# Kernel tuning notes

Measured on AMD Instinct MI355X. Metric: run time of the kernel, lower is better.

Reference implementation:

```python
import jax, jax.numpy as jnp
import numpy as np
import math

D_MODEL = 1024
HEADS = 16
D_K = D_MODEL // HEADS
D_FF = 2048
EPS = 1e-6


def layer_norm(x, alpha, bias):
    # torch.std uses unbiased estimator (ddof=1)
    m = x.mean(axis=-1, keepdims=True)
    var = ((x - m) ** 2).sum(axis=-1, keepdims=True) / (x.shape[-1] - 1)
    return alpha * (x - m) / (jnp.sqrt(var) + EPS) + bias


def setup_inputs() -> dict:
    key = jax.random.key(0)
    ks = jax.random.split(key, 12)
    s = 1.0 / math.sqrt(D_MODEL)
    return {
        "x": jax.random.normal(ks[0], (2, 2048, D_MODEL), dtype=jnp.float32),
        "mask": jnp.ones((2, 1, 1, 2048), dtype=jnp.float32),
        "Wq": jax.random.uniform(ks[1], (D_MODEL, D_MODEL), minval=-s, maxval=s),
        "Wk": jax.random.uniform(ks[2], (D_MODEL, D_MODEL), minval=-s, maxval=s),
        "Wv": jax.random.uniform(ks[3], (D_MODEL, D_MODEL), minval=-s, maxval=s),
        "Wo": jax.random.uniform(ks[4], (D_MODEL, D_MODEL), minval=-s, maxval=s),
        "bo": jnp.zeros((D_MODEL,), dtype=jnp.float32),
        "W1": jax.random.uniform(ks[5], (D_MODEL, D_FF), minval=-s, maxval=s),
        "b1": jnp.zeros((D_FF,), dtype=jnp.float32),
        "W2": jax.random.uniform(ks[6], (D_FF, D_MODEL), minval=-1.0 / math.sqrt(D_FF), maxval=1.0 / math.sqrt(D_FF)),
        "b2": jnp.zeros((D_MODEL,), dtype=jnp.float32),
        "ln1_a": jnp.ones((D_MODEL,), dtype=jnp.float32),
        "ln1_b": jnp.zeros((D_MODEL,), dtype=jnp.float32),
        "ln2_a": jnp.ones((D_MODEL,), dtype=jnp.float32),
        "ln2_b": jnp.zeros((D_MODEL,), dtype=jnp.float32),
    }


def reference(x, mask, Wq, Wk, Wv, Wo, bo, W1, b1, W2, b2, ln1_a, ln1_b, ln2_a, ln2_b):
    B, S, _ = x.shape
    # --- attention sublayer (pre-LN) ---
    x2 = layer_norm(x, ln1_a, ln1_b)
    q = (x2 @ Wq).reshape(B, S, HEADS, D_K).transpose(0, 2, 1, 3)  # [B,H,S,dk]
    k = (x2 @ Wk).reshape(B, S, HEADS, D_K).transpose(0, 2, 1, 3)
    v = (x2 @ Wv).reshape(B, S, HEADS, D_K).transpose(0, 2, 1, 3)
    attn = jnp.einsum("bhqd,bhkd->bhqk", q, k) / math.sqrt(D_K)
    attn = attn * mask                                  # multiplicative mask
    attn = jnp.where(attn == 0.0, -jnp.inf, attn)       # masked_fill(==0, -inf)
    scores = jax.nn.softmax(attn, axis=-1)
    av = jnp.einsum("bhqk,bhkd->bhqd", scores, v)
    concat = av.transpose(0, 2, 1, 3).reshape(B, S, D_MODEL)
    x = x + (concat @ Wo + bo)
    # --- FFN sublayer (pre-LN) ---
    x2 = layer_norm(x, ln2_a, ln2_b)
    h = jax.nn.relu(x2 @ W1 + b1)
    x = x + (h @ W2 + b2)
    return x
```

## Files before the change

### kernel.cpp

```cpp
#include <hip/hip_runtime.h>
#include <hip/hip_bf16.h>

typedef unsigned short u16;
typedef __attribute__((ext_vector_type(4))) float f32x4;
typedef __attribute__((ext_vector_type(8))) short bf16x8;

#define SEQ 2048
#define DM 1024
#define DKK 64
#define NH 16
#define DFF 2048
#define TOK 4096

#define AS1 __attribute__((address_space(1)))
#define AS3 __attribute__((address_space(3)))

#define MFMA16(a, b, c) __builtin_amdgcn_mfma_f32_16x16x32_bf16((a), (b), (c), 0, 0, 0)

__device__ __forceinline__ u16 f2b(float f) {
  unsigned u = __float_as_uint(f);
  u = u + 0x7fffu + ((u >> 16) & 1u);
  return (u16)(u >> 16);
}

__device__ __forceinline__ unsigned pk2(float lo, float hi) {
  union { __hip_bfloat162 h; unsigned u; } cv;
  cv.h = __float22bfloat162_rn(make_float2(lo, hi));
  return cv.u;
}

__device__ __forceinline__ void gload_lds16(const u16* g, u16* l) {
  __builtin_amdgcn_global_load_lds((AS1 unsigned*)(size_t)g, (AS3 unsigned*)l, 16, 0, 0);
}

__global__ __launch_bounds__(256)
void transpose_all(const float* __restrict__ Wq, const float* __restrict__ Wk,
                   const float* __restrict__ Wv, const float* __restrict__ Wo,
                   const float* __restrict__ W1, const float* __restrict__ W2,
                   u16* __restrict__ Wqkt, u16* __restrict__ Wvt, u16* __restrict__ Wot,
                   u16* __restrict__ W1t, u16* __restrict__ W2t) {
  const int bid = blockIdx.x;
  const float* src;
  u16* dst;
  int K, N, lb;
  if (bid < 1024)      { src = Wq; dst = Wqkt;                 K = 1024; N = 1024; lb = bid; }
  else if (bid < 2048) { src = Wk; dst = Wqkt + (1 << 20);     K = 1024; N = 1024; lb = bid - 1024; }
  else if (bid < 3072) { src = Wv; dst = Wvt;                  K = 1024; N = 1024; lb = bid - 2048; }
  else if (bid < 4096) { src = Wo; dst = Wot;                  K = 1024; N = 1024; lb = bid - 3072; }
  else if (bid < 6144) { src = W1; dst = W1t;                  K = 1024; N = 2048; lb = bid - 4096; }
  else                 { src = W2; dst = W2t;                  K = 2048; N = 1024; lb = bid - 6144; }
  const int nx = N / 32;
  const int n0 = (lb % nx) * 32, k0 = (lb / nx) * 32;
  __shared__ float t[32][33];
  const int tx = threadIdx.x, ty = threadIdx.y;
#pragma unroll
  for (int i = 0; i < 4; i++) {
    int k = ty + i * 8;
    t[k][tx] = src[(size_t)(k0 + k) * N + n0 + tx];
  }
  __syncthreads();
#pragma unroll
  for (int i = 0; i < 4; i++) {
    int n = ty + i * 8;
    dst[(size_t)(n0 + n) * K + k0 + tx] = f2b(t[tx][n]);
  }
}

__global__ __launch_bounds__(256)
void ln_kernel(const float* __restrict__ x, const float* __restrict__ alpha,
               const float* __restrict__ beta, u16* __restrict__ out) {
  const int row = blockIdx.x;
  const float4 v = ((const float4*)(x + (size_t)row * DM))[threadIdx.x];
  float s = v.x + v.y + v.z + v.w;
  float q = v.x * v.x + v.y * v.y + v.z * v.z + v.w * v.w;
#pragma unroll
  for (int off = 1; off < 64; off <<= 1) {
    s += __shfl_xor(s, off);
    q += __shfl_xor(q, off);
  }
  __shared__ float ss[4], qq[4];
  const int wid = threadIdx.x >> 6;
  if ((threadIdx.x & 63) == 0) { ss[wid] = s; qq[wid] = q; }
  __syncthreads();
  s = ss[0] + ss[1] + ss[2] + ss[3];
  q = qq[0] + qq[1] + qq[2] + qq[3];
  const float mean = s * (1.f / DM);
  float var = (q - (float)DM * mean * mean) * (1.f / (DM - 1));
  var = fmaxf(var, 0.f);
  const float inv = 1.f / (sqrtf(var) + 1e-6f);
  const float4 a4 = ((const float4*)alpha)[threadIdx.x];
  const float4 b4 = ((const float4*)beta)[threadIdx.x];
  ushort4 o;
  o.x = f2b((v.x - mean) * inv * a4.x + b4.x);
  o.y = f2b((v.y - mean) * inv * a4.y + b4.y);
  o.z = f2b((v.z - mean) * inv * a4.z + b4.z);
  o.w = f2b((v.w - mean) * inv * a4.w + b4.w);
  ((ushort4*)(out + (size_t)row * DM))[threadIdx.x] = o;
}

template <int MODE, int BM, int BN>
__global__ __launch_bounds__(256, 2)
void gemm_bt(const u16* __restrict__ A, const u16* __restrict__ Bt,
             int M, int N, int K,
             const float* __restrict__ bias, const float* __restrict__ res,
             void* __restrict__ outp, float oscale) {
  constexpr int AccM = BM / 32;
  constexpr int AccN = BN / 32;
  __shared__ alignas(16) u16 As[2][BM * 32];
  __shared__ alignas(16) u16 Bs[2][BN * 32];
  const int bm = blockIdx.x * BM, bn = blockIdx.y * BN;
  const int tid = threadIdx.x;
  const int lane = tid & 63, w = tid >> 6;
  const int wm = (w >> 1) * (BM / 2), wn = (w & 1) * (BN / 2);
  const int r = lane & 15, g = lane >> 4;
  const int srow = tid >> 2, skk = (tid & 3) * 8;

  f32x4 acc[AccM][AccN];
#pragma unroll
  for (int i = 0; i < AccM; i++)
#pragma unroll
    for (int j = 0; j < AccN; j++) acc[i][j] = (f32x4){0.f, 0.f, 0.f, 0.f};

  const u16* aP = A + (size_t)(bm + srow) * K + skk;
  const u16* bP = Bt + (size_t)(bn + srow) * K + skk;

  auto stage = [&](int kt, int buf) {
    gload_lds16(aP + kt, &As[buf][0] + w * 512);
    if (BM == 128) gload_lds16(aP + (size_t)64 * K + kt, &As[buf][0] + w * 512 + 2048);
    gload_lds16(bP + kt, &Bs[buf][0] + w * 512);
    if (BN == 128) gload_lds16(bP + (size_t)64 * K + kt, &Bs[buf][0] + w * 512 + 2048);
  };

  stage(0, 0);
  __syncthreads();

  const int NKT = K / 32;
  for (int it = 0; it < NKT; ++it) {
    const int buf = it & 1;
    if (it + 1 < NKT) stage((it + 1) * 32, buf ^ 1);
    bf16x8 af[AccM], bfr[AccN];
#pragma unroll
    for (int i = 0; i < AccM; i++) af[i] = *(const bf16x8*)(&As[buf][(wm + i * 16 + r) * 32 + g * 8]);
#pragma unroll
    for (int j = 0; j < AccN; j++) bfr[j] = *(const bf16x8*)(&Bs[buf][(wn + j * 16 + r) * 32 + g * 8]);
#pragma unroll
    for (int i = 0; i < AccM; i++)
#pragma unroll
      for (int j = 0; j < AccN; j++) acc[i][j] = MFMA16(af[i], bfr[j], acc[i][j]);
    __syncthreads();
  }

#pragma unroll
  for (int i = 0; i < AccM; i++)
#pragma unroll
    for (int j = 0; j < AccN; j++)
#pragma unroll
      for (int t = 0; t < 4; t++) {
        const int mg = bm + wm + i * 16 + g * 4 + t;
        const int ng = bn + wn + j * 16 + r;
        const float v = acc[i][j][t];
        if (MODE == 0) {
          const int which = ng >> 10, col = ng & 1023;
          const int bb = mg >> 11, ssx = mg & 2047, hh = col >> 6, dd = col & 63;
          const float sc = which ? 1.f : oscale;
          ((u16*)outp)[(size_t)which * (TOK * (size_t)DM) +
                       ((size_t)(bb * NH + hh) * SEQ + ssx) * DKK + dd] = f2b(v * sc);
        } else if (MODE == 1) {
          const int hh = mg >> 6, dd = mg & 63, bb = ng >> 11, ssx = ng & 2047;
          ((u16*)outp)[((size_t)(bb * NH + hh) * DKK + dd) * SEQ + ssx] = f2b(v);
        } else if (MODE == 2) {
          ((float*)outp)[(size_t)mg * N + ng] = res[(size_t)mg * N + ng] + v + bias[ng];
        } else {
          const float hv = v + bias[ng];
          ((u16*)outp)[(size_t)mg * N + ng] = f2b(hv > 0.f ? hv : 0.f);
        }
      }
}

__global__ __launch_bounds__(256, 4)
void attn_kernel(const u16* __restrict__ Q, const u16* __restrict__ Kb,
                 const u16* __restrict__ Vt, const float* __restrict__ mask,
                 u16* __restrict__ outc) {
  const int bid = blockIdx.x;
  const int bh = (bid & 7) * 4 + ((bid >> 3) & 3);
  const int qt = bid >> 5;
  const int b = bh >> 4, h = bh & 15;
  const int tid = threadIdx.x, lane = tid & 63, w = tid >> 6;
  const int r = lane & 15, g = lane >> 4;
  const int qbase = qt * 64 + w * 16;
  const u16* Qp = Q + ((size_t)bh * SEQ + qbase) * DKK;
  const u16* Kp = Kb + (size_t)bh * SEQ * DKK;
  const u16* Vp = Vt + (size_t)bh * DKK * SEQ;
  const float* mk = mask + b * SEQ;

  const bf16x8 bq0 = *(const bf16x8*)(Qp + r * DKK + g * 8);
  const bf16x8 bq1 = *(const bf16x8*)(Qp + r * DKK + 32 + g * 8);

  __shared__ __align__(16) u16 Ks[2][32 * 64];
  __shared__ __align__(16) u16 Vs[2][64 * 32];

  const int krow = w * 8 + (lane >> 3);
  const int kgr = (lane & 7) ^ (krow & 7);
  const u16* kSrc = Kp + (size_t)krow * DKK + kgr * 8;
  const int vrow = w * 16 + (lane >> 2);
  const int vgr = (lane & 3) ^ ((vrow >> 1) & 3);
  const u16* vSrc = Vp + (size_t)vrow * SEQ + vgr * 8;

  f32x4 o[4];
#pragma unroll
  for (int i = 0; i < 4; i++) o[i] = (f32x4){0.f, 0.f, 0.f, 0.f};
  float lr = 0.f;

  const int keyr = r & 7;

  gload_lds16(kSrc, &Ks[0][0] + w * 512);
  gload_lds16(vSrc, &Vs[0][0] + w * 512);
  asm volatile("s_waitcnt vmcnt(0)" ::: "memory");
  __builtin_amdgcn_s_barrier();

  const int NT = SEQ / 32;
  for (int it = 0; it < NT; ++it) {
    const int buf = it & 1;
    if (it + 1 < NT) {
      const int nsk = (it + 1) * 32;
      gload_lds16(kSrc + (size_t)nsk * DKK, &Ks[buf ^ 1][0] + w * 512);
      gload_lds16(vSrc + nsk, &Vs[buf ^ 1][0] + w * 512);
    }

    const bf16x8 ka0 = *(const bf16x8*)&Ks[buf][r * 64 + ((g ^ keyr) << 3)];
    const bf16x8 ka1 = *(const bf16x8*)&Ks[buf][r * 64 + (((g + 4) ^ keyr) << 3)];
    const bf16x8 kb0 = *(const bf16x8*)&Ks[buf][(16 + r) * 64 + ((g ^ keyr) << 3)];
    const bf16x8 kb1 = *(const bf16x8*)&Ks[buf][(16 + r) * 64 + (((g + 4) ^ keyr) << 3)];

    f32x4 s0 = (f32x4){0.f, 0.f, 0.f, 0.f};
    f32x4 s1 = (f32x4){0.f, 0.f, 0.f, 0.f};
    s0 = MFMA16(ka0, bq0, s0);
    s0 = MFMA16(ka1, bq1, s0);
    s1 = MFMA16(kb0, bq0, s1);
    s1 = MFMA16(kb1, bq1, s1);

    const int sk = it * 32;
    const float4 m0 = *(const float4*)(mk + sk + 4 * g);
    const float4 m1 = *(const float4*)(mk + sk + 16 + 4 * g);
    float p[8];
    p[0] = s0[0] * m0.x; p[1] = s0[1] * m0.y; p[2] = s0[2] * m0.z; p[3] = s0[3] * m0.w;
    p[4] = s1[0] * m1.x; p[5] = s1[1] * m1.y; p[6] = s1[2] * m1.z; p[7] = s1[3] * m1.w;
    float rs = 0.f;
#pragma unroll
    for (int t = 0; t < 8; t++) {
      p[t] = (p[t] == 0.f) ? 0.f : exp2f(p[t]);
      rs += p[t];
    }
    rs += __shfl_xor(rs, 16);
    rs += __shfl_xor(rs, 32);
    lr += rs;

    const unsigned w0 = pk2(p[0], p[1]), w1 = pk2(p[2], p[3]);
    const unsigned w2 = pk2(p[4], p[5]), w3 = pk2(p[6], p[7]);
    union { unsigned u[4]; bf16x8 v; } pu;
#pragma unroll
    for (int c = 0; c < 4; c++) {
      const int srcl = r + ((g & 1) * 2 + (c >> 1)) * 16;
      const unsigned lo = __shfl((c & 1) ? w1 : w0, srcl);
      const unsigned hi = __shfl((c & 1) ? w3 : w2, srcl);
      pu.u[c] = (g < 2) ? lo : hi;
    }
    const bf16x8 pa = pu.v;

#pragma unroll
    for (int dc = 0; dc < 4; dc++) {
      const int vr = dc * 16 + r;
      const bf16x8 bv = *(const bf16x8*)&Vs[buf][vr * 32 + ((g ^ ((vr >> 1) & 3)) << 3)];
      o[dc] = MFMA16(pa, bv, o[dc]);
    }

    asm volatile("s_waitcnt vmcnt(0)" ::: "memory");
    __builtin_amdgcn_s_barrier();
  }

  float lq[4];
#pragma unroll
  for (int t = 0; t < 4; t++) lq[t] = __shfl(lr, 4 * g + t);
#pragma unroll
  for (int dc = 0; dc < 4; dc++)
#pragma unroll
    for (int t = 0; t < 4; t++) {
      const int srow_g = qbase + g * 4 + t;
      outc[((size_t)(b * SEQ + srow_g)) * DM + h * DKK + dc * 16 + r] = f2b(o[dc][t] / lq[t]);
    }
}

extern "C" void kernel_launch(void* const* d_in, const int* in_sizes, int n_in,
                              void* d_out, int out_size, void* d_ws, size_t ws_size,
                              hipStream_t stream) {
  const float* x    = (const float*)d_in[0];
  const float* mask = (const float*)d_in[1];
  const float* Wq   = (const float*)d_in[2];
  const float* Wk   = (const float*)d_in[3];
  const float* Wv   = (const float*)d_in[4];
  const float* Wo   = (const float*)d_in[5];
  const float* bo   = (const float*)d_in[6];
  const float* W1   = (const float*)d_in[7];
  const float* b1   = (const float*)d_in[8];
  const float* W2   = (const float*)d_in[9];
  const float* b2   = (const float*)d_in[10];
  const float* l1a  = (const float*)d_in[11];
  const float* l1b  = (const float*)d_in[12];
  const float* l2a  = (const float*)d_in[13];
  const float* l2b  = (const float*)d_in[14];

  char* wsb = (char*)d_ws;
  u16* Wqkt = (u16*)(wsb + (0ull << 20));
  u16* Wvt  = (u16*)(wsb + (4ull << 20));
  u16* Wot  = (u16*)(wsb + (6ull << 20));
  u16* W1t  = (u16*)(wsb + (8ull << 20));
  u16* W2t  = (u16*)(wsb + (12ull << 20));
  u16* x2   = (u16*)(wsb + (16ull << 20));
  u16* qkb  = (u16*)(wsb + (24ull << 20));
  u16* vtb  = (u16*)(wsb + (40ull << 20));
  float* x1 = (float*)(wsb + (48ull << 20));
  u16* concat = x2;
  u16* x2b = qkb;
  u16* hb  = (u16*)(wsb + (32ull << 20));

  const float qscale = 0.125f * 1.4426950408889634f;

  transpose_all<<<dim3(8192), dim3(32, 8), 0, stream>>>(Wq, Wk, Wv, Wo, W1, W2,
                                                        Wqkt, Wvt, Wot, W1t, W2t);

  ln_kernel<<<TOK, 256, 0, stream>>>(x, l1a, l1b, x2);

  gemm_bt<0, 128, 128><<<dim3(TOK / 128, 2048 / 128), 256, 0, stream>>>(
      x2, Wqkt, TOK, 2048, DM, nullptr, nullptr, qkb, qscale);
  gemm_bt<1, 64, 128><<<dim3(DM / 64, TOK / 128), 256, 0, stream>>>(
      Wvt, x2, DM, TOK, DM, nullptr, nullptr, vtb, 1.0f);

  attn_kernel<<<dim3(1024), 256, 0, stream>>>(qkb, qkb + (size_t)TOK * DM, vtb, mask, concat);

  gemm_bt<2, 128, 64><<<dim3(TOK / 128, DM / 64), 256, 0, stream>>>(
      concat, Wot, TOK, DM, DM, bo, x, x1, 1.0f);

  ln_kernel<<<TOK, 256, 0, stream>>>(x1, l2a, l2b, x2b);

  gemm_bt<3, 128, 128><<<dim3(TOK / 128, DFF / 128), 256, 0, stream>>>(
      x2b, W1t, TOK, DFF, DM, b1, nullptr, hb, 1.0f);
  gemm_bt<2, 128, 64><<<dim3(TOK / 128, DM / 64), 256, 0, stream>>>(
      hb, W2t, TOK, DM, DFF, b2, x1, (float*)d_out, 1.0f);
}
```

Measured before the change: 251.7 us.

## Triple-buffer GEMM k-loop and widen attention key tile to 64

The GEMM moves from a double-buffered loop with __syncthreads to a three-stage LDS ring that prefetches two k-tiles ahead and uses a partial vmcnt wait, so global loads overlap more compute. The attention kernel processes 64 keys per iteration instead of 32, halving the number of barriers and loop trips. It also adds s_setprio around the MFMA sections, uses the raw exp2 builtin, and packs to bf16 with inline v_cvt_pk_bf16_f32. LDS use grows in both kernels, which can lower occupancy, and the hand-written waitcnt values must match the exact number of issued loads.

Result: faster. 228.5 us (-9.2%).

```diff
diff --git a/kernel.cpp b/kernel.cpp
--- a/kernel.cpp
+++ b/kernel.cpp
@@ -23,10 +23,10 @@
   return (u16)(u >> 16);
 }
 
-__device__ __forceinline__ unsigned pk2(float lo, float hi) {
-  union { __hip_bfloat162 h; unsigned u; } cv;
-  cv.h = __float22bfloat162_rn(make_float2(lo, hi));
-  return cv.u;
+__device__ __forceinline__ unsigned cvtpk(float lo, float hi) {
+  unsigned r;
+  asm("v_cvt_pk_bf16_f32 %0, %1, %2" : "=v"(r) : "v"(lo), "v"(hi));
+  return r;
 }
 
 __device__ __forceinline__ void gload_lds16(const u16* g, u16* l) {
@@ -106,8 +106,9 @@
              void* __restrict__ outp, float oscale) {
   constexpr int AccM = BM / 32;
   constexpr int AccN = BN / 32;
-  __shared__ alignas(16) u16 As[2][BM * 32];
-  __shared__ alignas(16) u16 Bs[2][BN * 32];
+  constexpr int L = (BM == 128 ? 2 : 1) + (BN == 128 ? 2 : 1);
+  __shared__ alignas(16) u16 As[3][BM * 32];
+  __shared__ alignas(16) u16 Bs[3][BN * 32];
   const int bm = blockIdx.x * BM, bn = blockIdx.y * BN;
   const int tid = threadIdx.x;
   const int lane = tid & 63, w = tid >> 6;
@@ -130,25 +131,41 @@
     gload_lds16(bP + kt, &Bs[buf][0] + w * 512);
     if (BN == 128) gload_lds16(bP + (size_t)64 * K + kt, &Bs[buf][0] + w * 512 + 2048);
   };
-
+  auto waitL = [&]() {
+    if constexpr (L == 4) asm volatile("s_waitcnt vmcnt(4) lgkmcnt(0)" ::: "memory");
+    else if constexpr (L == 3) asm volatile("s_waitcnt vmcnt(3) lgkmcnt(0)" ::: "memory");
+    else asm volatile("s_waitcnt vmcnt(2) lgkmcnt(0)" ::: "memory");
+  };
+  auto compute = [&](int buf) {
+    bf16x8 af[AccM], bfr[AccN];
+#pragma unroll
+    for (int i = 0; i < AccM; i++) af[i] = *(const bf16x8*)(&As[buf][(wm + i * 16 + r) * 32 + g * 8]);
+#pragma unroll
+    for (int j = 0; j < AccN; j++) bfr[j] = *(const bf16x8*)(&Bs[buf][(wn + j * 16 + r) * 32 + g * 8]);
+#pragma unroll
+    for (int i = 0; i < AccM; i++)
+#pragma unroll
+      for (int j = 0; j < AccN; j++) acc[i][j] = MFMA16(af[i], bfr[j], acc[i][j]);
+  };
+
+  const int NKT = K / 32;
   stage(0, 0);
-  __syncthreads();
-
-  const int NKT = K / 32;
-  for (int it = 0; it < NKT; ++it) {
-    const int buf = it & 1;
-    if (it + 1 < NKT) stage((it + 1) * 32, buf ^ 1);
-    bf16x8 af[AccM], bfr[AccN];
-#pragma unroll
-    for (int i = 0; i < AccM; i++) af[i] = *(const bf16x8*)(&As[buf][(wm + i * 16 + r) * 32 + g * 8]);
-#pragma unroll
-    for (int j = 0; j < AccN; j++) bfr[j] = *(const bf16x8*)(&Bs[buf][(wn + j * 16 + r) * 32 + g * 8]);
-#pragma unroll
-    for (int i = 0; i < AccM; i++)
-#pragma unroll
-      for (int j = 0; j < AccN; j++) acc[i][j] = MFMA16(af[i], bfr[j], acc[i][j]);
-    __syncthreads();
-  }
+  stage(32, 1);
+  waitL();
+  __builtin_amdgcn_s_barrier();
+  __builtin_amdgcn_sched_barrier(0);
+  for (int it = 0; it < NKT - 2; ++it) {
+    stage((it + 2) * 32, (it + 2) % 3);
+    compute(it % 3);
+    waitL();
+    __builtin_amdgcn_s_barrier();
+    __builtin_amdgcn_sched_barrier(0);
+  }
+  compute((NKT - 2) % 3);
+  asm volatile("s_waitcnt vmcnt(0) lgkmcnt(0)" ::: "memory");
+  __builtin_amdgcn_s_barrier();
+  __builtin_amdgcn_sched_barrier(0);
+  compute((NKT - 1) % 3);
 
 #pragma unroll
   for (int i = 0; i < AccM; i++)
@@ -196,86 +213,111 @@
   const bf16x8 bq0 = *(const bf16x8*)(Qp + r * DKK + g * 8);
   const bf16x8 bq1 = *(const bf16x8*)(Qp + r * DKK + 32 + g * 8);
 
-  __shared__ __align__(16) u16 Ks[2][32 * 64];
-  __shared__ __align__(16) u16 Vs[2][64 * 32];
-
-  const int krow = w * 8 + (lane >> 3);
-  const int kgr = (lane & 7) ^ (krow & 7);
-  const u16* kSrc = Kp + (size_t)krow * DKK + kgr * 8;
-  const int vrow = w * 16 + (lane >> 2);
-  const int vgr = (lane & 3) ^ ((vrow >> 1) & 3);
-  const u16* vSrc = Vp + (size_t)vrow * SEQ + vgr * 8;
+  __shared__ __align__(16) u16 Ks[2][64 * 64];
+  __shared__ __align__(16) u16 Vs[2][64 * 64];
+
+  const int srow8 = lane >> 3;
+  const int sgr = (lane & 7) ^ srow8;
+  const u16* kSrc1 = Kp + (size_t)(w * 16 + srow8) * DKK + sgr * 8;
+  const u16* kSrc2 = kSrc1 + 8 * DKK;
+  const u16* vSrc1 = Vp + (size_t)(w * 16 + srow8) * SEQ + sgr * 8;
+  const u16* vSrc2 = vSrc1 + 8 * SEQ;
 
   f32x4 o[4];
 #pragma unroll
   for (int i = 0; i < 4; i++) o[i] = (f32x4){0.f, 0.f, 0.f, 0.f};
   float lr = 0.f;
-
   const int keyr = r & 7;
 
-  gload_lds16(kSrc, &Ks[0][0] + w * 512);
-  gload_lds16(vSrc, &Vs[0][0] + w * 512);
+  gload_lds16(kSrc1, &Ks[0][0] + w * 1024);
+  gload_lds16(kSrc2, &Ks[0][0] + w * 1024 + 512);
+  gload_lds16(vSrc1, &Vs[0][0] + w * 1024);
+  gload_lds16(vSrc2, &Vs[0][0] + w * 1024 + 512);
   asm volatile("s_waitcnt vmcnt(0)" ::: "memory");
   __builtin_amdgcn_s_barrier();
-
-  const int NT = SEQ / 32;
+  __builtin_amdgcn_sched_barrier(0);
+
+  const int NT = SEQ / 64;
   for (int it = 0; it < NT; ++it) {
     const int buf = it & 1;
     if (it + 1 < NT) {
-      const int nsk = (it + 1) * 32;
-      gload_lds16(kSrc + (size_t)nsk * DKK, &Ks[buf ^ 1][0] + w * 512);
-      gload_lds16(vSrc + nsk, &Vs[buf ^ 1][0] + w * 512);
-    }
-
-    const bf16x8 ka0 = *(const bf16x8*)&Ks[buf][r * 64 + ((g ^ keyr) << 3)];
-    const bf16x8 ka1 = *(const bf16x8*)&Ks[buf][r * 64 + (((g + 4) ^ keyr) << 3)];
-    const bf16x8 kb0 = *(const bf16x8*)&Ks[buf][(16 + r) * 64 + ((g ^ keyr) << 3)];
-    const bf16x8 kb1 = *(const bf16x8*)&Ks[buf][(16 + r) * 64 + (((g + 4) ^ keyr) << 3)];
-
-    f32x4 s0 = (f32x4){0.f, 0.f, 0.f, 0.f};
-    f32x4 s1 = (f32x4){0.f, 0.f, 0.f, 0.f};
-    s0 = MFMA16(ka0, bq0, s0);
-    s0 = MFMA16(ka1, bq1, s0);
-    s1 = MFMA16(kb0, bq0, s1);
-    s1 = MFMA16(kb1, bq1, s1);
-
-    const int sk = it * 32;
-    const float4 m0 = *(const float4*)(mk + sk + 4 * g);
-    const float4 m1 = *(const float4*)(mk + sk + 16 + 4 * g);
-    float p[8];
-    p[0] = s0[0] * m0.x; p[1] = s0[1] * m0.y; p[2] = s0[2] * m0.z; p[3] = s0[3] * m0.w;
-    p[4] = s1[0] * m1.x; p[5] = s1[1] * m1.y; p[6] = s1[2] * m1.z; p[7] = s1[3] * m1.w;
+      const int nsk = (it + 1) * 64;
+      u16* kd = &Ks[buf ^ 1][0] + w * 1024;
+      gload_lds16(kSrc1 + (size_t)nsk * DKK, kd);
+      gload_lds16(kSrc2 + (size_t)nsk * DKK, kd + 512);
+      u16* vd = &Vs[buf ^ 1][0] + w * 1024;
+      gload_lds16(vSrc1 + nsk, vd);
+      gload_lds16(vSrc2 + nsk, vd + 512);
+    }
+
+    f32x4 s[4];
+    __builtin_amdgcn_s_setprio(1);
+#pragma unroll
+    for (int ks = 0; ks < 4; ks++) {
+      const bf16x8 ka0 = *(const bf16x8*)&Ks[buf][(ks * 16 + r) * 64 + ((g ^ keyr) << 3)];
+      const bf16x8 ka1 = *(const bf16x8*)&Ks[buf][(ks * 16 + r) * 64 + (((g + 4) ^ keyr) << 3)];
+      f32x4 z = (f32x4){0.f, 0.f, 0.f, 0.f};
+      z = MFMA16(ka0, bq0, z);
+      z = MFMA16(ka1, bq1, z);
+      s[ks] = z;
+    }
+    __builtin_amdgcn_s_setprio(0);
+
+    const int sk = it * 64;
+    float p[16];
     float rs = 0.f;
 #pragma unroll
-    for (int t = 0; t < 8; t++) {
-      p[t] = (p[t] == 0.f) ? 0.f : exp2f(p[t]);
-      rs += p[t];
+    for (int ks = 0; ks < 4; ks++) {
+      const float4 mm = *(const float4*)(mk + sk + ks * 16 + 4 * g);
+      float pr0 = s[ks][0] * mm.x, pr1 = s[ks][1] * mm.y;
+      float pr2 = s[ks][2] * mm.z, pr3 = s[ks][3] * mm.w;
+      float e0 = __builtin_amdgcn_exp2f(pr0), e1 = __builtin_amdgcn_exp2f(pr1);
+      float e2 = __builtin_amdgcn_exp2f(pr2), e3 = __builtin_amdgcn_exp2f(pr3);
+      e0 = (pr0 == 0.f) ? 0.f : e0;
+      e1 = (pr1 == 0.f) ? 0.f : e1;
+      e2 = (pr2 == 0.f) ? 0.f : e2;
+      e3 = (pr3 == 0.f) ? 0.f : e3;
+      p[ks * 4 + 0] = e0; p[ks * 4 + 1] = e1; p[ks * 4 + 2] = e2; p[ks * 4 + 3] = e3;
+      rs += e0 + e1 + e2 + e3;
     }
     rs += __shfl_xor(rs, 16);
     rs += __shfl_xor(rs, 32);
     lr += rs;
 
-    const unsigned w0 = pk2(p[0], p[1]), w1 = pk2(p[2], p[3]);
-    const unsigned w2 = pk2(p[4], p[5]), w3 = pk2(p[6], p[7]);
-    union { unsigned u[4]; bf16x8 v; } pu;
-#pragma unroll
-    for (int c = 0; c < 4; c++) {
-      const int srcl = r + ((g & 1) * 2 + (c >> 1)) * 16;
-      const unsigned lo = __shfl((c & 1) ? w1 : w0, srcl);
-      const unsigned hi = __shfl((c & 1) ? w3 : w2, srcl);
-      pu.u[c] = (g < 2) ? lo : hi;
-    }
-    const bf16x8 pa = pu.v;
-
+    unsigned wk[4][2];
+#pragma unroll
+    for (int ks = 0; ks < 4; ks++) {
+      wk[ks][0] = cvtpk(p[ks * 4 + 0], p[ks * 4 + 1]);
+      wk[ks][1] = cvtpk(p[ks * 4 + 2], p[ks * 4 + 3]);
+    }
+    bf16x8 pa[2];
+#pragma unroll
+    for (int hh2 = 0; hh2 < 2; hh2++) {
+      union { unsigned u[4]; bf16x8 v; } pu;
+#pragma unroll
+      for (int c = 0; c < 4; c++) {
+        const int srcl = r + ((g & 1) * 2 + (c >> 1)) * 16;
+        const unsigned lo = __shfl(wk[2 * hh2][c & 1], srcl);
+        const unsigned hi = __shfl(wk[2 * hh2 + 1][c & 1], srcl);
+        pu.u[c] = (g < 2) ? lo : hi;
+      }
+      pa[hh2] = pu.v;
+    }
+
+    __builtin_amdgcn_s_setprio(1);
 #pragma unroll
     for (int dc = 0; dc < 4; dc++) {
       const int vr = dc * 16 + r;
-      const bf16x8 bv = *(const bf16x8*)&Vs[buf][vr * 32 + ((g ^ ((vr >> 1) & 3)) << 3)];
-      o[dc] = MFMA16(pa, bv, o[dc]);
-    }
-
-    asm volatile("s_waitcnt vmcnt(0)" ::: "memory");
+      const bf16x8 bv0 = *(const bf16x8*)&Vs[buf][vr * 64 + ((g ^ keyr) << 3)];
+      const bf16x8 bv1 = *(const bf16x8*)&Vs[buf][vr * 64 + (((g + 4) ^ keyr) << 3)];
+      o[dc] = MFMA16(pa[0], bv0, o[dc]);
+      o[dc] = MFMA16(pa[1], bv1, o[dc]);
+    }
+    __builtin_amdgcn_s_setprio(0);
+
+    asm volatile("s_waitcnt vmcnt(0) lgkmcnt(0)" ::: "memory");
     __builtin_amdgcn_s_barrier();
+    __builtin_amdgcn_sched_barrier(0);
   }
 
   float lq[4];
```
